# Kernel tuning notes

Hardware: AMD Instinct MI355X
Metric: run time of the kernel (lower is better)

## Reference

```python
import jax, jax.numpy as jnp
import numpy as np

B, S, T = 16384, 64, 64
I, M, H = 4, 16, 64  # input_dim, middle_dim, hidden_dim


def _cell(x, h, c, Wih, Whh, b):
    # PyTorch LSTM cell, gate order i, f, g, o; b = b_ih + b_hh
    gates = x @ Wih.T + h @ Whh.T + b
    i, f, g, o = jnp.split(gates, 4, axis=-1)
    c = jax.nn.sigmoid(f) * c + jax.nn.sigmoid(i) * jnp.tanh(g)
    h = jax.nn.sigmoid(o) * jnp.tanh(c)
    return h, c


def setup_inputs() -> dict:
    key = jax.random.key(0)
    ks = jax.random.split(key, 18)
    p = lambda k, shape: (jax.random.uniform(k, shape, jnp.float32) - 0.5) * 0.25
    return {
        "src": jax.random.normal(ks[0], (B, S, I), jnp.float32),
        "trg": jax.random.normal(ks[1], (B, T, I), jnp.float32),
        "W_in": p(ks[2], (M, I)), "b_in": p(ks[3], (M,)),
        "enc_Wih0": p(ks[4], (4 * H, M)), "enc_Whh0": p(ks[5], (4 * H, H)), "enc_b0": p(ks[6], (4 * H,)),
        "enc_Wih1": p(ks[7], (4 * H, H)), "enc_Whh1": p(ks[8], (4 * H, H)), "enc_b1": p(ks[9], (4 * H,)),
        "dec_Wih0": p(ks[10], (4 * H, M)), "dec_Whh0": p(ks[11], (4 * H, H)), "dec_b0": p(ks[12], (4 * H,)),
        "dec_Wih1": p(ks[13], (4 * H, H)), "dec_Whh1": p(ks[14], (4 * H, H)), "dec_b1": p(ks[15], (4 * H,)),
        "W_out": p(ks[16], (I, H)), "b_out": p(ks[17], (I,)),
    }


def reference(src, trg, W_in, b_in,
              enc_Wih0, enc_Whh0, enc_b0, enc_Wih1, enc_Whh1, enc_b1,
              dec_Wih0, dec_Whh0, dec_b0, dec_Wih1, dec_Whh1, dec_b1,
              W_out, b_out):
    b = src.shape[0]
    dt = src.dtype

    def layer_scan(xs, Wih, Whh, bb):
        # xs: [S, B, D] -> ys: [S, B, H], final (h, c)
        h0 = jnp.zeros((b, H), dt)
        def step(carry, x):
            h, c = carry
            h, c = _cell(x, h, c, Wih, Whh, bb)
            return (h, c), h
        (h, c), ys = jax.lax.scan(step, (h0, h0), xs)
        return ys, h, c

    # encoder: fc_in then 2-layer LSTM (dropout inactive in eval)
    mid = src @ W_in.T + b_in                      # [B, S, M]
    ys1, h1, c1 = layer_scan(mid.transpose(1, 0, 2), enc_Wih0, enc_Whh0, enc_b0)
    _, h2, c2 = layer_scan(ys1, enc_Wih1, enc_Whh1, enc_b1)

    # stepwise decoder, teacher_forcing_ratio=0 branch: next input = pred + trg[:, t-1]
    def dec_step(carry, trg_t):
        h1, c1, h2, c2, x = carry
        m = x @ W_in.T + b_in                      # [B, M]
        h1, c1 = _cell(m, h1, c1, dec_Wih0, dec_Whh0, dec_b0)
        h2, c2 = _cell(h1, h2, c2, dec_Wih1, dec_Whh1, dec_b1)
        pred = h2 @ W_out.T + b_out                # [B, I]
        return (h1, c1, h2, c2, pred + trg_t), pred

    init = (h1, c1, h2, c2, trg[:, 0])
    _, preds = jax.lax.scan(dec_step, init, trg.transpose(1, 0, 2))  # [T, B, I]
    return preds.transpose(1, 0, 2) + trg
```

## Files before the change

### kernel.cpp

```cpp
#include <hip/hip_runtime.h>

typedef __bf16 bf16x8 __attribute__((ext_vector_type(8)));
typedef float  f32x4  __attribute__((ext_vector_type(4)));

__device__ __forceinline__ unsigned short f2bf(float x){
  unsigned int u = __float_as_uint(x);
  u += 0x7fffu + ((u >> 16) & 1u);
  return (unsigned short)(u >> 16);
}
__device__ __forceinline__ float sigm(float x){
  return __builtin_amdgcn_rcpf(1.0f + __builtin_amdgcn_exp2f(-1.44269504f * x));
}
__device__ __forceinline__ float tanh_(float x){
  return fmaf(-2.0f, __builtin_amdgcn_rcpf(1.0f + __builtin_amdgcn_exp2f(2.88539008f * x)), 1.0f);
}

__global__ void pack_weights(const float* __restrict__ eWih0, const float* __restrict__ eWhh0,
                             const float* __restrict__ eWih1, const float* __restrict__ eWhh1,
                             const float* __restrict__ dWih0, const float* __restrict__ dWhh0,
                             const float* __restrict__ dWih1, const float* __restrict__ dWhh1,
                             const float* __restrict__ Wout,
                             unsigned short* __restrict__ out){
  int t = blockIdx.x * 256 + threadIdx.x;
  if (t >= 226 * 64) return;
  int lane = t & 63;
  int f    = t >> 6;
  unsigned short vals[8];
  if (f >= 224){
    int kt = f - 224, n = lane & 15;
#pragma unroll
    for (int jj = 0; jj < 8; jj++){
      int k = kt * 32 + (lane >> 4) * 8 + jj;
      vals[jj] = (n < 4) ? f2bf(Wout[n * 64 + k]) : (unsigned short)0;
    }
  } else {
    const float *Wih, *Whh; int kx, ntile, kt;
    if (f < 48)       { Wih=eWih0; Whh=eWhh0; kx=16; ntile=f/3;        kt=f%3; }
    else if (f < 112) { Wih=eWih1; Whh=eWhh1; kx=64; ntile=(f-48)/4;   kt=(f-48)%4; }
    else if (f < 160) { Wih=dWih0; Whh=dWhh0; kx=16; ntile=(f-112)/3;  kt=(f-112)%3; }
    else              { Wih=dWih1; Whh=dWhh1; kx=64; ntile=(f-160)/4;  kt=(f-160)%4; }
    int n    = ntile * 16 + (lane & 15);
    int hoff = (kx == 16) ? 32 : 64;
#pragma unroll
    for (int jj = 0; jj < 8; jj++){
      int k = kt * 32 + (lane >> 4) * 8 + jj;
      float v;
      if (k < kx)        v = Wih[n * kx + k];
      else if (k < hoff) v = 0.0f;
      else               v = Whh[n * 64 + (k - hoff)];
      vals[jj] = f2bf(v);
    }
  }
  uint4 o;
  o.x = (unsigned)vals[0] | ((unsigned)vals[1] << 16);
  o.y = (unsigned)vals[2] | ((unsigned)vals[3] << 16);
  o.z = (unsigned)vals[4] | ((unsigned)vals[5] << 16);
  o.w = (unsigned)vals[6] | ((unsigned)vals[7] << 16);
  ((uint4*)out)[f * 64 + lane] = o;
}

__device__ __forceinline__ void write_h(unsigned short* buf, int k, int quad,
                                        const unsigned short* h){
  unsigned short* p = buf + (((k >> 5) * 64) + quad * 4 + (((k >> 3) & 3) << 4)) * 8 + (k & 7);
#pragma unroll
  for (int e = 0; e < 4; e++) p[e * 8] = h[e];
}

__device__ __forceinline__ void load_frags(const unsigned short* __restrict__ pw,
                                           int base0, int base1, int w, int lane,
                                           bf16x8 (&B0)[3][4], bf16x8 (&B1)[4][4]){
#pragma unroll
  for (int g = 0; g < 4; g++){
    int nt = 4 * g + w;
#pragma unroll
    for (int kt = 0; kt < 3; kt++)
      B0[kt][g] = *(const bf16x8*)(pw + (((long)(base0 + nt * 3 + kt)) * 64 + lane) * 8);
#pragma unroll
    for (int kt = 0; kt < 4; kt++)
      B1[kt][g] = *(const bf16x8*)(pw + (((long)(base1 + nt * 4 + kt)) * 64 + lane) * 8);
  }
}

template<int KT, int SZ>
__device__ __forceinline__ void cell_compute(const unsigned short* __restrict__ A,
                                             const bf16x8 (&B)[KT][4],
                                             const float (&bias)[4],
                                             float (&c)[8],
                                             unsigned short (&hout)[8],
                                             int lane){
  f32x4 acc[4][2];
#pragma unroll
  for (int g = 0; g < 4; g++){
    f32x4 b = {bias[g], bias[g], bias[g], bias[g]};
    acc[g][0] = b; acc[g][1] = b;
  }
#pragma unroll
  for (int kt = 0; kt < KT; kt++){
    bf16x8 a0 = *(const bf16x8*)(A +      (kt * 64 + lane) * 8);
    bf16x8 a1 = *(const bf16x8*)(A + SZ + (kt * 64 + lane) * 8);
#pragma unroll
    for (int g = 0; g < 4; g++){
      acc[g][0] = __builtin_amdgcn_mfma_f32_16x16x32_bf16(a0, B[kt][g], acc[g][0], 0, 0, 0);
      acc[g][1] = __builtin_amdgcn_mfma_f32_16x16x32_bf16(a1, B[kt][g], acc[g][1], 0, 0, 0);
    }
  }
#pragma unroll
  for (int rt = 0; rt < 2; rt++){
#pragma unroll
    for (int e = 0; e < 4; e++){
      float is = sigm(acc[0][rt][e]);
      float fs = sigm(acc[1][rt][e]);
      float gt = tanh_(acc[2][rt][e]);
      float os = sigm(acc[3][rt][e]);
      int idx = rt * 4 + e;
      c[idx] = fmaf(fs, c[idx], is * gt);
      hout[idx] = f2bf(os * tanh_(c[idx]));
    }
  }
}

__global__ __launch_bounds__(256, 2)
void lstm_main(const float* __restrict__ src, const float* __restrict__ trg,
               const float* __restrict__ W_in, const float* __restrict__ b_in,
               const float* __restrict__ eb0, const float* __restrict__ eb1,
               const float* __restrict__ db0, const float* __restrict__ db1,
               const float* __restrict__ bout,
               const unsigned short* __restrict__ pw,
               float* __restrict__ out){
  __shared__ __align__(16) unsigned short A0[2][2][1536];
  __shared__ __align__(16) unsigned short A1[2][2][2048];
  __shared__ __align__(16) float xsrc[2][128];
  __shared__ __align__(16) float xfb[128];
  __shared__ __align__(16) unsigned short sWoutF[1024];

  const int tid  = threadIdx.x;
  const int lane = tid & 63;
  const int w    = tid >> 6;
  const int quad = lane >> 4;
  const int l16  = lane & 15;
  const int j    = 16 * w + l16;
  const int rowg0 = blockIdx.x * 32;
  const int mm   = tid & 15;
  const int xr   = tid >> 4;

  {
    uint4 z; z.x = z.y = z.z = z.w = 0u;
    uint4* a0p = (uint4*)A0;
    uint4* a1p = (uint4*)A1;
    for (int i = tid; i < 768;  i += 256) a0p[i] = z;
    for (int i = tid; i < 1024; i += 256) a1p[i] = z;
    if (tid < 128) ((uint4*)sWoutF)[tid] = ((const uint4*)pw)[224 * 64 + tid];
    if (tid < 128) xsrc[0][tid] = src[(long)(rowg0 + (tid >> 2)) * 256 + (tid & 3)];
  }
  const float4 wv = *(const float4*)&W_in[mm * 4];
  const float  bin = b_in[mm];

  bf16x8 B0[3][4], B1[4][4];
  float bias0[4], bias1[4];
  float c0[8] = {0,0,0,0,0,0,0,0}, c1[8] = {0,0,0,0,0,0,0,0};
  load_frags(pw, 0, 48, w, lane, B0, B1);
#pragma unroll
  for (int g = 0; g < 4; g++){ int n = 64*g + j; bias0[g] = eb0[n]; bias1[g] = eb1[n]; }
  __syncthreads();

  unsigned short h0r[8], h1r[8];
  const int xoff = (xr | ((mm >> 3) << 4)) * 8 + (mm & 7);

  for (int t = 0; t < 64; t++){
    int cur = t & 1, nxt = cur ^ 1;
    float xv;
    if (tid < 128)
      xv = src[(long)(rowg0 + (tid >> 2)) * 256 + ((t == 63 ? 63 : t + 1) << 2) + (tid & 3)];
    {
      float4 x0 = *(const float4*)&xsrc[cur][xr * 4];
      float4 x1 = *(const float4*)&xsrc[cur][(xr + 16) * 4];
      float m0 = bin + x0.x*wv.x + x0.y*wv.y + x0.z*wv.z + x0.w*wv.w;
      float m1 = bin + x1.x*wv.x + x1.y*wv.y + x1.z*wv.z + x1.w*wv.w;
      A0[cur][0][xoff] = f2bf(m0);
      A0[cur][1][xoff] = f2bf(m1);
    }
    if (tid < 128) xsrc[nxt][tid] = xv;
    __syncthreads();
    cell_compute<3, 1536>(&A0[cur][0][0], B0, bias0, c0, h0r, lane);
#pragma unroll
    for (int rt = 0; rt < 2; rt++){
      write_h(&A0[nxt][rt][0], 32 + j, quad, h0r + rt * 4);
      write_h(&A1[cur][rt][0],      j, quad, h0r + rt * 4);
    }
    if (t > 0){
      cell_compute<4, 2048>(&A1[nxt][0][0], B1, bias1, c1, h1r, lane);
#pragma unroll
      for (int rt = 0; rt < 2; rt++)
        write_h(&A1[cur][rt][0], 64 + j, quad, h1r + rt * 4);
    }
  }
  __syncthreads();
  cell_compute<4, 2048>(&A1[1][0][0], B1, bias1, c1, h1r, lane);
#pragma unroll
  for (int rt = 0; rt < 2; rt++)
    write_h(&A1[0][rt][0], 64 + j, quad, h1r + rt * 4);

  load_frags(pw, 112, 160, w, lane, B0, B1);
#pragma unroll
  for (int g = 0; g < 4; g++){ int n = 64*g + j; bias0[g] = db0[n]; bias1[g] = db1[n]; }
  const float bo = (w < 2 && l16 < 4) ? bout[l16] : 0.0f;
  if (tid < 128) xfb[tid] = trg[(long)(rowg0 + (tid >> 2)) * 256 + (tid & 3)];
  __syncthreads();

  for (int t = 0; t < 64; t++){
    int cur = t & 1, nxt = cur ^ 1;
    float tpre[4];
    if (w < 2 && l16 < 4){
#pragma unroll
      for (int e = 0; e < 4; e++)
        tpre[e] = trg[(long)(rowg0 + w * 16 + quad * 4 + e) * 256 + t * 4 + l16];
    }
    {
      float4 x0 = *(const float4*)&xfb[xr * 4];
      float4 x1 = *(const float4*)&xfb[(xr + 16) * 4];
      float m0 = bin + x0.x*wv.x + x0.y*wv.y + x0.z*wv.z + x0.w*wv.w;
      float m1 = bin + x1.x*wv.x + x1.y*wv.y + x1.z*wv.z + x1.w*wv.w;
      A0[cur][0][xoff] = f2bf(m0);
      A0[cur][1][xoff] = f2bf(m1);
    }
    __syncthreads();
    cell_compute<3, 1536>(&A0[cur][0][0], B0, bias0, c0, h0r, lane);
#pragma unroll
    for (int rt = 0; rt < 2; rt++){
      write_h(&A0[nxt][rt][0], 32 + j, quad, h0r + rt * 4);
      write_h(&A1[cur][rt][0],      j, quad, h0r + rt * 4);
    }
    __syncthreads();
    cell_compute<4, 2048>(&A1[cur][0][0], B1, bias1, c1, h1r, lane);
#pragma unroll
    for (int rt = 0; rt < 2; rt++)
      write_h(&A1[nxt][rt][0], 64 + j, quad, h1r + rt * 4);
    __syncthreads();
    if (w < 2){
      const unsigned short* Ah = &A1[nxt][w][0];
      bf16x8 a2 = *(const bf16x8*)(Ah + (2 * 64 + lane) * 8);
      bf16x8 a3 = *(const bf16x8*)(Ah + (3 * 64 + lane) * 8);
      bf16x8 bw0 = *(const bf16x8*)(sWoutF + lane * 8);
      bf16x8 bw1 = *(const bf16x8*)(sWoutF + 512 + lane * 8);
      f32x4 po = {bo, bo, bo, bo};
      po = __builtin_amdgcn_mfma_f32_16x16x32_bf16(a2, bw0, po, 0, 0, 0);
      po = __builtin_amdgcn_mfma_f32_16x16x32_bf16(a3, bw1, po, 0, 0, 0);
      if (l16 < 4){
#pragma unroll
        for (int e = 0; e < 4; e++){
          int row = w * 16 + quad * 4 + e;
          float v = po[e] + tpre[e];
          out[(long)(rowg0 + row) * 256 + t * 4 + l16] = v;
          xfb[row * 4 + l16] = v;
        }
      }
    }
    __syncthreads();
  }
}

extern "C" void kernel_launch(void* const* d_in, const int* in_sizes, int n_in,
                              void* d_out, int out_size, void* d_ws, size_t ws_size,
                              hipStream_t stream){
  (void)n_in; (void)out_size; (void)ws_size;
  const float* src   = (const float*)d_in[0];
  const float* trg   = (const float*)d_in[1];
  const float* W_in  = (const float*)d_in[2];
  const float* b_in  = (const float*)d_in[3];
  const float* eWih0 = (const float*)d_in[4];
  const float* eWhh0 = (const float*)d_in[5];
  const float* eb0   = (const float*)d_in[6];
  const float* eWih1 = (const float*)d_in[7];
  const float* eWhh1 = (const float*)d_in[8];
  const float* eb1   = (const float*)d_in[9];
  const float* dWih0 = (const float*)d_in[10];
  const float* dWhh0 = (const float*)d_in[11];
  const float* db0   = (const float*)d_in[12];
  const float* dWih1 = (const float*)d_in[13];
  const float* dWhh1 = (const float*)d_in[14];
  const float* db1   = (const float*)d_in[15];
  const float* Wout  = (const float*)d_in[16];
  const float* bout  = (const float*)d_in[17];
  unsigned short* pw = (unsigned short*)d_ws;

  pack_weights<<<57, 256, 0, stream>>>(eWih0, eWhh0, eWih1, eWhh1,
                                       dWih0, dWhh0, dWih1, dWhh1, Wout, pw);

  int B    = in_sizes[0] / 256;
  int nblk = B / 32;
  lstm_main<<<nblk, 256, 0, stream>>>(src, trg, W_in, b_in, eb0, eb1, db0, db1,
                                      bout, pw, (float*)d_out);
}
```

Baseline: 498.7 us.

## Fold decoder output feedback into layer-0 weights to drop a sync per step

Precomputes dWih0·W_in·W_out as extra K tiles so decoder layer 0 consumes the previous h2 directly instead of waiting for the prediction, and folds b_out into the input bias. The output projection is deferred by one step and overlapped, removing one block barrier per decoder step and the xfb feedback buffer. In exchange, layer 0 does more MFMA work, holds more weight registers, and accumulates a slightly different bf16 rounding of the composite matrix.

```diff
diff --git a/kernel.cpp b/kernel.cpp
--- a/kernel.cpp
+++ b/kernel.cpp
@@ -19,26 +19,42 @@
                              const float* __restrict__ eWih1, const float* __restrict__ eWhh1,
                              const float* __restrict__ dWih0, const float* __restrict__ dWhh0,
                              const float* __restrict__ dWih1, const float* __restrict__ dWhh1,
-                             const float* __restrict__ Wout,
+                             const float* __restrict__ W_in,  const float* __restrict__ Wout,
                              unsigned short* __restrict__ out){
   int t = blockIdx.x * 256 + threadIdx.x;
-  if (t >= 226 * 64) return;
+  if (t >= 258 * 64) return;
   int lane = t & 63;
   int f    = t >> 6;
   unsigned short vals[8];
-  if (f >= 224){
-    int kt = f - 224, n = lane & 15;
+  if (f >= 256){
+    int kt = f - 256, n = lane & 15;
 #pragma unroll
     for (int jj = 0; jj < 8; jj++){
       int k = kt * 32 + (lane >> 4) * 8 + jj;
       vals[jj] = (n < 4) ? f2bf(Wout[n * 64 + k]) : (unsigned short)0;
+    }
+  } else if (f >= 112 && f < 192 && ((f - 112) % 5) >= 3){
+    int ntile = (f - 112) / 5, kt = (f - 112) % 5;
+    int n = ntile * 16 + (lane & 15);
+#pragma unroll
+    for (int jj = 0; jj < 8; jj++){
+      int k2 = (kt - 3) * 32 + (lane >> 4) * 8 + jj;
+      float s = 0.0f;
+#pragma unroll
+      for (int m = 0; m < 16; m++){
+        float wf = 0.0f;
+#pragma unroll
+        for (int i = 0; i < 4; i++) wf = fmaf(W_in[m * 4 + i], Wout[i * 64 + k2], wf);
+        s = fmaf(dWih0[n * 16 + m], wf, s);
+      }
+      vals[jj] = f2bf(s);
     }
   } else {
     const float *Wih, *Whh; int kx, ntile, kt;
     if (f < 48)       { Wih=eWih0; Whh=eWhh0; kx=16; ntile=f/3;        kt=f%3; }
     else if (f < 112) { Wih=eWih1; Whh=eWhh1; kx=64; ntile=(f-48)/4;   kt=(f-48)%4; }
-    else if (f < 160) { Wih=dWih0; Whh=dWhh0; kx=16; ntile=(f-112)/3;  kt=(f-112)%3; }
-    else              { Wih=dWih1; Whh=dWhh1; kx=64; ntile=(f-160)/4;  kt=(f-160)%4; }
+    else if (f < 192) { Wih=dWih0; Whh=dWhh0; kx=16; ntile=(f-112)/5;  kt=(f-112)%5; }
+    else              { Wih=dWih1; Whh=dWhh1; kx=64; ntile=(f-192)/4;  kt=(f-192)%4; }
     int n    = ntile * 16 + (lane & 15);
     int hoff = (kx == 16) ? 32 : 64;
 #pragma unroll
@@ -66,15 +82,16 @@
   for (int e = 0; e < 4; e++) p[e * 8] = h[e];
 }
 
+template<int KT0>
 __device__ __forceinline__ void load_frags(const unsigned short* __restrict__ pw,
                                            int base0, int base1, int w, int lane,
-                                           bf16x8 (&B0)[3][4], bf16x8 (&B1)[4][4]){
+                                           bf16x8 (*B0)[4], bf16x8 (*B1)[4]){
 #pragma unroll
   for (int g = 0; g < 4; g++){
     int nt = 4 * g + w;
 #pragma unroll
-    for (int kt = 0; kt < 3; kt++)
-      B0[kt][g] = *(const bf16x8*)(pw + (((long)(base0 + nt * 3 + kt)) * 64 + lane) * 8);
+    for (int kt = 0; kt < KT0; kt++)
+      B0[kt][g] = *(const bf16x8*)(pw + (((long)(base0 + nt * KT0 + kt)) * 64 + lane) * 8);
 #pragma unroll
     for (int kt = 0; kt < 4; kt++)
       B1[kt][g] = *(const bf16x8*)(pw + (((long)(base1 + nt * 4 + kt)) * 64 + lane) * 8);
@@ -83,10 +100,10 @@
 
 template<int KT, int SZ>
 __device__ __forceinline__ void cell_compute(const unsigned short* __restrict__ A,
-                                             const bf16x8 (&B)[KT][4],
-                                             const float (&bias)[4],
-                                             float (&c)[8],
-                                             unsigned short (&hout)[8],
+                                             const bf16x8 (*B)[4],
+                                             const float* bias,
+                                             float* c,
+                                             unsigned short* hout,
                                              int lane){
   f32x4 acc[4][2];
 #pragma unroll
@@ -127,10 +144,9 @@
                const float* __restrict__ bout,
                const unsigned short* __restrict__ pw,
                float* __restrict__ out){
-  __shared__ __align__(16) unsigned short A0[2][2][1536];
+  __shared__ __align__(16) unsigned short A0[2][2][2560];
   __shared__ __align__(16) unsigned short A1[2][2][2048];
   __shared__ __align__(16) float xsrc[2][128];
-  __shared__ __align__(16) float xfb[128];
   __shared__ __align__(16) unsigned short sWoutF[1024];
 
   const int tid  = threadIdx.x;
@@ -147,18 +163,18 @@
     uint4 z; z.x = z.y = z.z = z.w = 0u;
     uint4* a0p = (uint4*)A0;
     uint4* a1p = (uint4*)A1;
-    for (int i = tid; i < 768;  i += 256) a0p[i] = z;
+    for (int i = tid; i < 1280; i += 256) a0p[i] = z;
     for (int i = tid; i < 1024; i += 256) a1p[i] = z;
-    if (tid < 128) ((uint4*)sWoutF)[tid] = ((const uint4*)pw)[224 * 64 + tid];
+    if (tid < 128) ((uint4*)sWoutF)[tid] = ((const uint4*)pw)[256 * 64 + tid];
     if (tid < 128) xsrc[0][tid] = src[(long)(rowg0 + (tid >> 2)) * 256 + (tid & 3)];
   }
   const float4 wv = *(const float4*)&W_in[mm * 4];
   const float  bin = b_in[mm];
 
-  bf16x8 B0[3][4], B1[4][4];
+  bf16x8 B0[5][4], B1[4][4];
   float bias0[4], bias1[4];
   float c0[8] = {0,0,0,0,0,0,0,0}, c1[8] = {0,0,0,0,0,0,0,0};
-  load_frags(pw, 0, 48, w, lane, B0, B1);
+  load_frags<3>(pw, 0, 48, w, lane, B0, B1);
 #pragma unroll
   for (int g = 0; g < 4; g++){ int n = 64*g + j; bias0[g] = eb0[n]; bias1[g] = eb1[n]; }
   __syncthreads();
@@ -181,7 +197,7 @@
     }
     if (tid < 128) xsrc[nxt][tid] = xv;
     __syncthreads();
-    cell_compute<3, 1536>(&A0[cur][0][0], B0, bias0, c0, h0r, lane);
+    cell_compute<3, 2560>(&A0[cur][0][0], B0, bias0, c0, h0r, lane);
 #pragma unroll
     for (int rt = 0; rt < 2; rt++){
       write_h(&A0[nxt][rt][0], 32 + j, quad, h0r + rt * 4);
@@ -197,65 +213,88 @@
   __syncthreads();
   cell_compute<4, 2048>(&A1[1][0][0], B1, bias1, c1, h1r, lane);
 #pragma unroll
-  for (int rt = 0; rt < 2; rt++)
+  for (int rt = 0; rt < 2; rt++){
     write_h(&A1[0][rt][0], 64 + j, quad, h1r + rt * 4);
-
-  load_frags(pw, 112, 160, w, lane, B0, B1);
+    write_h(&A0[0][rt][0], 96 + j, quad, h1r + rt * 4);
+  }
+
+  load_frags<5>(pw, 112, 192, w, lane, B0, B1);
 #pragma unroll
   for (int g = 0; g < 4; g++){ int n = 64*g + j; bias0[g] = db0[n]; bias1[g] = db1[n]; }
   const float bo = (w < 2 && l16 < 4) ? bout[l16] : 0.0f;
-  if (tid < 128) xfb[tid] = trg[(long)(rowg0 + (tid >> 2)) * 256 + (tid & 3)];
-  __syncthreads();
+  float bq = bin;
+#pragma unroll
+  for (int i = 0; i < 4; i++) bq = fmaf(bout[i], ((const float*)&wv)[i], bq);
+  {
+    float4 x0 = *(const float4*)&trg[(long)(rowg0 + xr) * 256];
+    float4 x1 = *(const float4*)&trg[(long)(rowg0 + xr + 16) * 256];
+    float m0 = bin + x0.x*wv.x + x0.y*wv.y + x0.z*wv.z + x0.w*wv.w;
+    float m1 = bin + x1.x*wv.x + x1.y*wv.y + x1.z*wv.z + x1.w*wv.w;
+    A0[0][0][xoff] = f2bf(m0);
+    A0[0][1][xoff] = f2bf(m1);
+  }
 
   for (int t = 0; t < 64; t++){
     int cur = t & 1, nxt = cur ^ 1;
-    float tpre[4];
-    if (w < 2 && l16 < 4){
-#pragma unroll
-      for (int e = 0; e < 4; e++)
-        tpre[e] = trg[(long)(rowg0 + w * 16 + quad * 4 + e) * 256 + t * 4 + l16];
-    }
     {
-      float4 x0 = *(const float4*)&xfb[xr * 4];
-      float4 x1 = *(const float4*)&xfb[(xr + 16) * 4];
-      float m0 = bin + x0.x*wv.x + x0.y*wv.y + x0.z*wv.z + x0.w*wv.w;
-      float m1 = bin + x1.x*wv.x + x1.y*wv.y + x1.z*wv.z + x1.w*wv.w;
-      A0[cur][0][xoff] = f2bf(m0);
-      A0[cur][1][xoff] = f2bf(m1);
+      float4 x0 = *(const float4*)&trg[(long)(rowg0 + xr) * 256 + t * 4];
+      float4 x1 = *(const float4*)&trg[(long)(rowg0 + xr + 16) * 256 + t * 4];
+      float m0 = bq + x0.x*wv.x + x0.y*wv.y + x0.z*wv.z + x0.w*wv.w;
+      float m1 = bq + x1.x*wv.x + x1.y*wv.y + x1.z*wv.z + x1.w*wv.w;
+      A0[nxt][0][xoff] = f2bf(m0);
+      A0[nxt][1][xoff] = f2bf(m1);
     }
     __syncthreads();
-    cell_compute<3, 1536>(&A0[cur][0][0], B0, bias0, c0, h0r, lane);
+    cell_compute<5, 2560>(&A0[cur][0][0], B0, bias0, c0, h0r, lane);
 #pragma unroll
     for (int rt = 0; rt < 2; rt++){
       write_h(&A0[nxt][rt][0], 32 + j, quad, h0r + rt * 4);
       write_h(&A1[cur][rt][0],      j, quad, h0r + rt * 4);
     }
-    __syncthreads();
-    cell_compute<4, 2048>(&A1[cur][0][0], B1, bias1, c1, h1r, lane);
-#pragma unroll
-    for (int rt = 0; rt < 2; rt++)
-      write_h(&A1[nxt][rt][0], 64 + j, quad, h1r + rt * 4);
-    __syncthreads();
-    if (w < 2){
-      const unsigned short* Ah = &A1[nxt][w][0];
-      bf16x8 a2 = *(const bf16x8*)(Ah + (2 * 64 + lane) * 8);
-      bf16x8 a3 = *(const bf16x8*)(Ah + (3 * 64 + lane) * 8);
+    if (w < 2 && t > 0){
+      const unsigned short* Ah = &A0[cur][w][0];
+      bf16x8 a3  = *(const bf16x8*)(Ah + (3 * 64 + lane) * 8);
+      bf16x8 a4  = *(const bf16x8*)(Ah + (4 * 64 + lane) * 8);
       bf16x8 bw0 = *(const bf16x8*)(sWoutF + lane * 8);
       bf16x8 bw1 = *(const bf16x8*)(sWoutF + 512 + lane * 8);
       f32x4 po = {bo, bo, bo, bo};
-      po = __builtin_amdgcn_mfma_f32_16x16x32_bf16(a2, bw0, po, 0, 0, 0);
-      po = __builtin_amdgcn_mfma_f32_16x16x32_bf16(a3, bw1, po, 0, 0, 0);
+      po = __builtin_amdgcn_mfma_f32_16x16x32_bf16(a3, bw0, po, 0, 0, 0);
+      po = __builtin_amdgcn_mfma_f32_16x16x32_bf16(a4, bw1, po, 0, 0, 0);
       if (l16 < 4){
 #pragma unroll
         for (int e = 0; e < 4; e++){
           int row = w * 16 + quad * 4 + e;
-          float v = po[e] + tpre[e];
-          out[(long)(rowg0 + row) * 256 + t * 4 + l16] = v;
-          xfb[row * 4 + l16] = v;
+          out[(long)(rowg0 + row) * 256 + (t - 1) * 4 + l16] =
+              po[e] + trg[(long)(rowg0 + row) * 256 + (t - 1) * 4 + l16];
         }
       }
     }
     __syncthreads();
+    cell_compute<4, 2048>(&A1[cur][0][0], B1, bias1, c1, h1r, lane);
+#pragma unroll
+    for (int rt = 0; rt < 2; rt++){
+      write_h(&A1[nxt][rt][0], 64 + j, quad, h1r + rt * 4);
+      write_h(&A0[nxt][rt][0], 96 + j, quad, h1r + rt * 4);
+    }
+  }
+  __syncthreads();
+  if (w < 2){
+    const unsigned short* Ah = &A0[0][w][0];
+    bf16x8 a3  = *(const bf16x8*)(Ah + (3 * 64 + lane) * 8);
+    bf16x8 a4  = *(const bf16x8*)(Ah + (4 * 64 + lane) * 8);
+    bf16x8 bw0 = *(const bf16x8*)(sWoutF + lane * 8);
+    bf16x8 bw1 = *(const bf16x8*)(sWoutF + 512 + lane * 8);
+    f32x4 po = {bo, bo, bo, bo};
+    po = __builtin_amdgcn_mfma_f32_16x16x32_bf16(a3, bw0, po, 0, 0, 0);
+    po = __builtin_amdgcn_mfma_f32_16x16x32_bf16(a4, bw1, po, 0, 0, 0);
+    if (l16 < 4){
+#pragma unroll
+      for (int e = 0; e < 4; e++){
+        int row = w * 16 + quad * 4 + e;
+        out[(long)(rowg0 + row) * 256 + 63 * 4 + l16] =
+            po[e] + trg[(long)(rowg0 + row) * 256 + 63 * 4 + l16];
+      }
+    }
   }
 }
 
@@ -283,8 +322,9 @@
   const float* bout  = (const float*)d_in[17];
   unsigned short* pw = (unsigned short*)d_ws;
 
-  pack_weights<<<57, 256, 0, stream>>>(eWih0, eWhh0, eWih1, eWhh1,
-                                       dWih0, dWhh0, dWih1, dWhh1, Wout, pw);
+  pack_weights<<<65, 256, 0, stream>>>(eWih0, eWhh0, eWih1, eWhh1,
+                                       dWih0, dWhh0, dWih1, dWhh1,
+                                       W_in, Wout, pw);
 
   int B    = in_sizes[0] / 256;
   int nblk = B / 32;
```

Result: slower. 565.4 us (+13.4%).

## Fold output projection into decoder input and defer prediction to next step

Applied to the files above, without the earlier changes.

The decoder's feedback path (pred -> fc_in) is folded algebraically into a precomputed W_in·W_out matrix. The next step's layer-0 input is now computed directly from h2 with MFMA, and bias and teacher terms are preloaded from trg. Each prediction is written one step late at the top of the next iteration, which removes one __syncthreads and the separate output-projection phase per step. In exchange, each wave does redundant output MFMAs, pays extra global trg loads per step, and rounds the fused weight to bf16, which slightly changes the numerics.

```diff
diff --git a/kernel.cpp b/kernel.cpp
--- a/kernel.cpp
+++ b/kernel.cpp
@@ -19,14 +19,24 @@
                              const float* __restrict__ eWih1, const float* __restrict__ eWhh1,
                              const float* __restrict__ dWih0, const float* __restrict__ dWhh0,
                              const float* __restrict__ dWih1, const float* __restrict__ dWhh1,
-                             const float* __restrict__ Wout,
+                             const float* __restrict__ W_in,  const float* __restrict__ Wout,
                              unsigned short* __restrict__ out){
   int t = blockIdx.x * 256 + threadIdx.x;
-  if (t >= 226 * 64) return;
+  if (t >= 228 * 64) return;
   int lane = t & 63;
   int f    = t >> 6;
   unsigned short vals[8];
-  if (f >= 224){
+  if (f >= 226){
+    int kt = f - 226, n = lane & 15;
+#pragma unroll
+    for (int jj = 0; jj < 8; jj++){
+      int k = kt * 32 + (lane >> 4) * 8 + jj;
+      float s = 0.0f;
+#pragma unroll
+      for (int i = 0; i < 4; i++) s = fmaf(W_in[n * 4 + i], Wout[i * 64 + k], s);
+      vals[jj] = f2bf(s);
+    }
+  } else if (f >= 224){
     int kt = f - 224, n = lane & 15;
 #pragma unroll
     for (int jj = 0; jj < 8; jj++){
@@ -68,7 +78,7 @@
 
 __device__ __forceinline__ void load_frags(const unsigned short* __restrict__ pw,
                                            int base0, int base1, int w, int lane,
-                                           bf16x8 (&B0)[3][4], bf16x8 (&B1)[4][4]){
+                                           bf16x8 (*B0)[4], bf16x8 (*B1)[4]){
 #pragma unroll
   for (int g = 0; g < 4; g++){
     int nt = 4 * g + w;
@@ -81,12 +91,28 @@
   }
 }
 
+__device__ __forceinline__ void pointwise8(const f32x4 (&acc)[4][2], float* c,
+                                           unsigned short* h){
+#pragma unroll
+  for (int s = 0; s < 2; s++)
+#pragma unroll
+    for (int e = 0; e < 4; e++){
+      float is = sigm(acc[0][s][e]);
+      float fs = sigm(acc[1][s][e]);
+      float gt = tanh_(acc[2][s][e]);
+      float os = sigm(acc[3][s][e]);
+      int idx = s * 4 + e;
+      c[idx] = fmaf(fs, c[idx], is * gt);
+      h[idx] = f2bf(os * tanh_(c[idx]));
+    }
+}
+
 template<int KT, int SZ>
 __device__ __forceinline__ void cell_compute(const unsigned short* __restrict__ A,
-                                             const bf16x8 (&B)[KT][4],
-                                             const float (&bias)[4],
-                                             float (&c)[8],
-                                             unsigned short (&hout)[8],
+                                             const bf16x8 (*B)[4],
+                                             const float* bias,
+                                             float* c,
+                                             unsigned short* hout,
                                              int lane){
   f32x4 acc[4][2];
 #pragma unroll
@@ -104,19 +130,7 @@
       acc[g][1] = __builtin_amdgcn_mfma_f32_16x16x32_bf16(a1, B[kt][g], acc[g][1], 0, 0, 0);
     }
   }
-#pragma unroll
-  for (int rt = 0; rt < 2; rt++){
-#pragma unroll
-    for (int e = 0; e < 4; e++){
-      float is = sigm(acc[0][rt][e]);
-      float fs = sigm(acc[1][rt][e]);
-      float gt = tanh_(acc[2][rt][e]);
-      float os = sigm(acc[3][rt][e]);
-      int idx = rt * 4 + e;
-      c[idx] = fmaf(fs, c[idx], is * gt);
-      hout[idx] = f2bf(os * tanh_(c[idx]));
-    }
-  }
+  pointwise8(acc, c, hout);
 }
 
 __global__ __launch_bounds__(256, 2)
@@ -130,8 +144,6 @@
   __shared__ __align__(16) unsigned short A0[2][2][1536];
   __shared__ __align__(16) unsigned short A1[2][2][2048];
   __shared__ __align__(16) float xsrc[2][128];
-  __shared__ __align__(16) float xfb[128];
-  __shared__ __align__(16) unsigned short sWoutF[1024];
 
   const int tid  = threadIdx.x;
   const int lane = tid & 63;
@@ -149,10 +161,10 @@
     uint4* a1p = (uint4*)A1;
     for (int i = tid; i < 768;  i += 256) a0p[i] = z;
     for (int i = tid; i < 1024; i += 256) a1p[i] = z;
-    if (tid < 128) ((uint4*)sWoutF)[tid] = ((const uint4*)pw)[224 * 64 + tid];
     if (tid < 128) xsrc[0][tid] = src[(long)(rowg0 + (tid >> 2)) * 256 + (tid & 3)];
   }
   const float4 wv = *(const float4*)&W_in[mm * 4];
+  const float* wvp = (const float*)&wv;
   const float  bin = b_in[mm];
 
   bf16x8 B0[3][4], B1[4][4];
@@ -203,59 +215,147 @@
   load_frags(pw, 112, 160, w, lane, B0, B1);
 #pragma unroll
   for (int g = 0; g < 4; g++){ int n = 64*g + j; bias0[g] = db0[n]; bias1[g] = db1[n]; }
-  const float bo = (w < 2 && l16 < 4) ? bout[l16] : 0.0f;
-  if (tid < 128) xfb[tid] = trg[(long)(rowg0 + (tid >> 2)) * 256 + (tid & 3)];
+  bf16x8 WoF0 = *(const bf16x8*)(pw + ((long)224 * 64 + lane) * 8);
+  bf16x8 WoF1 = *(const bf16x8*)(pw + ((long)225 * 64 + lane) * 8);
+  bf16x8 WmF0 = *(const bf16x8*)(pw + ((long)226 * 64 + lane) * 8);
+  bf16x8 WmF1 = *(const bf16x8*)(pw + ((long)227 * 64 + lane) * 8);
+  const float bo = (l16 < 4) ? bout[l16] : 0.0f;
+  float bq = bin;
+#pragma unroll
+  for (int i = 0; i < 4; i++) bq = fmaf(bout[i], wvp[i], bq);
+#pragma unroll
+  for (int s = 0; s < 2; s++){
+    unsigned short mv[4];
+#pragma unroll
+    for (int e = 0; e < 4; e++){
+      const float4 x4 = *(const float4*)&trg[(long)(rowg0 + quad*4 + e + 16*s) * 256];
+      mv[e] = f2bf(bin + x4.x*wv.x + x4.y*wv.y + x4.z*wv.z + x4.w*wv.w);
+    }
+    write_h(&A0[0][s][0], mm, quad, mv);
+  }
+  float q_pref[8], trg_pref[8];
   __syncthreads();
 
   for (int t = 0; t < 64; t++){
-    int cur = t & 1, nxt = cur ^ 1;
-    float tpre[4];
-    if (w < 2 && l16 < 4){
-#pragma unroll
-      for (int e = 0; e < 4; e++)
-        tpre[e] = trg[(long)(rowg0 + w * 16 + quad * 4 + e) * 256 + t * 4 + l16];
-    }
-    {
-      float4 x0 = *(const float4*)&xfb[xr * 4];
-      float4 x1 = *(const float4*)&xfb[(xr + 16) * 4];
-      float m0 = bin + x0.x*wv.x + x0.y*wv.y + x0.z*wv.z + x0.w*wv.w;
-      float m1 = bin + x1.x*wv.x + x1.y*wv.y + x1.z*wv.z + x1.w*wv.w;
-      A0[cur][0][xoff] = f2bf(m0);
-      A0[cur][1][xoff] = f2bf(m1);
-    }
-    __syncthreads();
-    cell_compute<3, 1536>(&A0[cur][0][0], B0, bias0, c0, h0r, lane);
-#pragma unroll
-    for (int rt = 0; rt < 2; rt++){
-      write_h(&A0[nxt][rt][0], 32 + j, quad, h0r + rt * 4);
-      write_h(&A1[cur][rt][0],      j, quad, h0r + rt * 4);
-    }
-    __syncthreads();
-    cell_compute<4, 2048>(&A1[cur][0][0], B1, bias1, c1, h1r, lane);
-#pragma unroll
-    for (int rt = 0; rt < 2; rt++)
-      write_h(&A1[nxt][rt][0], 64 + j, quad, h1r + rt * 4);
-    __syncthreads();
-    if (w < 2){
-      const unsigned short* Ah = &A1[nxt][w][0];
-      bf16x8 a2 = *(const bf16x8*)(Ah + (2 * 64 + lane) * 8);
-      bf16x8 a3 = *(const bf16x8*)(Ah + (3 * 64 + lane) * 8);
-      bf16x8 bw0 = *(const bf16x8*)(sWoutF + lane * 8);
-      bf16x8 bw1 = *(const bf16x8*)(sWoutF + 512 + lane * 8);
-      f32x4 po = {bo, bo, bo, bo};
-      po = __builtin_amdgcn_mfma_f32_16x16x32_bf16(a2, bw0, po, 0, 0, 0);
-      po = __builtin_amdgcn_mfma_f32_16x16x32_bf16(a3, bw1, po, 0, 0, 0);
-      if (l16 < 4){
+    const int cur = t & 1, nxt = cur ^ 1;
+    unsigned short* A1c = &A1[cur][0][0];
+    unsigned short* A0c = &A0[cur][0][0];
+    bf16x8 ah2[2][2], ah01[2][2];
+#pragma unroll
+    for (int k2 = 0; k2 < 2; k2++)
+#pragma unroll
+      for (int s = 0; s < 2; s++){
+        ah2[k2][s]  = *(const bf16x8*)(A1c + s * 2048 + ((2 + k2) * 64 + lane) * 8);
+        ah01[k2][s] = *(const bf16x8*)(A0c + s * 1536 + ((1 + k2) * 64 + lane) * 8);
+      }
+    if (t > 0){
+      f32x4 po[2], macc[2];
+#pragma unroll
+      for (int s = 0; s < 2; s++){
+        f32x4 p = {bo, bo, bo, bo};
+        p = __builtin_amdgcn_mfma_f32_16x16x32_bf16(ah2[0][s], WoF0, p, 0, 0, 0);
+        p = __builtin_amdgcn_mfma_f32_16x16x32_bf16(ah2[1][s], WoF1, p, 0, 0, 0);
+        po[s] = p;
+        f32x4 q = {q_pref[s*4+0], q_pref[s*4+1], q_pref[s*4+2], q_pref[s*4+3]};
+        q = __builtin_amdgcn_mfma_f32_16x16x32_bf16(ah2[0][s], WmF0, q, 0, 0, 0);
+        q = __builtin_amdgcn_mfma_f32_16x16x32_bf16(ah2[1][s], WmF1, q, 0, 0, 0);
+        macc[s] = q;
+      }
+      if (w < 2 && l16 < 4){
 #pragma unroll
         for (int e = 0; e < 4; e++){
           int row = w * 16 + quad * 4 + e;
-          float v = po[e] + tpre[e];
-          out[(long)(rowg0 + row) * 256 + t * 4 + l16] = v;
-          xfb[row * 4 + l16] = v;
+          out[(long)(rowg0 + row) * 256 + (t - 1) * 4 + l16] = po[w][e] + trg_pref[w*4+e];
         }
       }
+#pragma unroll
+      for (int s = 0; s < 2; s++){
+        unsigned short mv[4];
+#pragma unroll
+        for (int e = 0; e < 4; e++) mv[e] = f2bf(macc[s][e]);
+        write_h(&A0[cur][s][0], mm, quad, mv);
+      }
+    }
+    bf16x8 a00[2];
+#pragma unroll
+    for (int s = 0; s < 2; s++) a00[s] = *(const bf16x8*)(A0c + s * 1536 + lane * 8);
+    f32x4 acc[4][2];
+#pragma unroll
+    for (int g = 0; g < 4; g++){
+      f32x4 b = {bias0[g], bias0[g], bias0[g], bias0[g]};
+      acc[g][0] = b; acc[g][1] = b;
+    }
+#pragma unroll
+    for (int g = 0; g < 4; g++)
+#pragma unroll
+      for (int s = 0; s < 2; s++){
+        acc[g][s] = __builtin_amdgcn_mfma_f32_16x16x32_bf16(ah01[0][s], B0[1][g], acc[g][s], 0, 0, 0);
+        acc[g][s] = __builtin_amdgcn_mfma_f32_16x16x32_bf16(ah01[1][s], B0[2][g], acc[g][s], 0, 0, 0);
+        acc[g][s] = __builtin_amdgcn_mfma_f32_16x16x32_bf16(a00[s],     B0[0][g], acc[g][s], 0, 0, 0);
+      }
+    pointwise8(acc, c0, h0r);
+#pragma unroll
+    for (int s = 0; s < 2; s++){
+      write_h(&A0[nxt][s][0], 32 + j, quad, h0r + s * 4);
+      write_h(&A1[cur][s][0],      j, quad, h0r + s * 4);
     }
     __syncthreads();
+    bf16x8 a1f[4][2];
+#pragma unroll
+    for (int kt = 0; kt < 4; kt++)
+#pragma unroll
+      for (int s = 0; s < 2; s++)
+        a1f[kt][s] = *(const bf16x8*)(A1c + s * 2048 + (kt * 64 + lane) * 8);
+    float4 t4[8];
+    float  tv[8];
+#pragma unroll
+    for (int s = 0; s < 2; s++)
+#pragma unroll
+      for (int e = 0; e < 4; e++){
+        long rb = (long)(rowg0 + quad * 4 + e + 16 * s) * 256 + t * 4;
+        t4[s*4+e] = *(const float4*)&trg[rb];
+        if (l16 < 4) tv[s*4+e] = trg[rb + l16];
+      }
+    f32x4 acc1[4][2];
+#pragma unroll
+    for (int g = 0; g < 4; g++){
+      f32x4 b = {bias1[g], bias1[g], bias1[g], bias1[g]};
+      acc1[g][0] = b; acc1[g][1] = b;
+    }
+#pragma unroll
+    for (int g = 0; g < 4; g++)
+#pragma unroll
+      for (int s = 0; s < 2; s++){
+        acc1[g][s] = __builtin_amdgcn_mfma_f32_16x16x32_bf16(a1f[2][s], B1[2][g], acc1[g][s], 0, 0, 0);
+        acc1[g][s] = __builtin_amdgcn_mfma_f32_16x16x32_bf16(a1f[3][s], B1[3][g], acc1[g][s], 0, 0, 0);
+        acc1[g][s] = __builtin_amdgcn_mfma_f32_16x16x32_bf16(a1f[0][s], B1[0][g], acc1[g][s], 0, 0, 0);
+        acc1[g][s] = __builtin_amdgcn_mfma_f32_16x16x32_bf16(a1f[1][s], B1[1][g], acc1[g][s], 0, 0, 0);
+      }
+    pointwise8(acc1, c1, h1r);
+#pragma unroll
+    for (int s = 0; s < 2; s++)
+      write_h(&A1[nxt][s][0], 64 + j, quad, h1r + s * 4);
+#pragma unroll
+    for (int i8 = 0; i8 < 8; i8++){
+      q_pref[i8] = bq + t4[i8].x*wv.x + t4[i8].y*wv.y + t4[i8].z*wv.z + t4[i8].w*wv.w;
+      trg_pref[i8] = tv[i8];
+    }
+    __syncthreads();
+  }
+  if (w < 2){
+    const int s = w;
+    bf16x8 x2 = *(const bf16x8*)(&A1[0][s][0] + (2 * 64 + lane) * 8);
+    bf16x8 x3 = *(const bf16x8*)(&A1[0][s][0] + (3 * 64 + lane) * 8);
+    f32x4 p = {bo, bo, bo, bo};
+    p = __builtin_amdgcn_mfma_f32_16x16x32_bf16(x2, WoF0, p, 0, 0, 0);
+    p = __builtin_amdgcn_mfma_f32_16x16x32_bf16(x3, WoF1, p, 0, 0, 0);
+    if (l16 < 4){
+#pragma unroll
+      for (int e = 0; e < 4; e++){
+        int row = s * 16 + quad * 4 + e;
+        out[(long)(rowg0 + row) * 256 + 252 + l16] = p[e] + trg_pref[s*4+e];
+      }
+    }
   }
 }
 
@@ -284,7 +384,8 @@
   unsigned short* pw = (unsigned short*)d_ws;
 
   pack_weights<<<57, 256, 0, stream>>>(eWih0, eWhh0, eWih1, eWhh1,
-                                       dWih0, dWhh0, dWih1, dWhh1, Wout, pw);
+                                       dWih0, dWhh0, dWih1, dWhh1,
+                                       W_in, Wout, pw);
 
   int B    = in_sizes[0] / 256;
   int nblk = B / 32;
```

Result: slower. 825.0 us (+65.4%).
